# Kernel tuning notes

Measured on AMD Instinct MI355X. Metric: run time of the kernel, lower is better.

## Reference

```python
import jax, jax.numpy as jnp
import numpy as np

N_HEADS = 32
N_KV_HEADS = 8
HEAD_DIM = 128
ROPE_BASE = 10000.0
NEG_INF = -1e9


def rope(x, base=ROPE_BASE, offset=0):
    # x: [B, H, L, d]; 'traditional' RoPE with the module's rotation formula.
    d = x.shape[-1]
    t = jnp.arange(x.shape[2], dtype=jnp.float32) + offset
    freqs = base ** (-jnp.arange(0, d, 2, dtype=jnp.float32) / d)  # [d/2]
    ang = t[:, None] * freqs[None, :]                              # [L, d/2]
    cos, sin = jnp.cos(ang), jnp.sin(ang)
    x1, x2 = x[..., 0::2], x[..., 1::2]
    out = jnp.stack([x1 * cos + x2 * sin, x1 * sin - x2 * cos], axis=-1)
    return out.reshape(x.shape)


def setup_inputs() -> dict:
    key = jax.random.key(0)
    ks = jax.random.split(key, 5)
    B, L, D = 2, 2048, 4096
    x = jax.random.normal(ks[0], (B, L, D), dtype=jnp.float32)
    wq = jax.random.normal(ks[1], (D, N_HEADS * HEAD_DIM), dtype=jnp.float32) * 0.02
    wk = jax.random.normal(ks[2], (D, N_KV_HEADS * HEAD_DIM), dtype=jnp.float32) * 0.02
    wv = jax.random.normal(ks[3], (D, N_KV_HEADS * HEAD_DIM), dtype=jnp.float32) * 0.02
    wo = jax.random.normal(ks[4], (N_HEADS * HEAD_DIM, D), dtype=jnp.float32) * 0.02
    # causal additive mask [L, L]
    mask = jnp.where(jnp.tril(jnp.ones((L, L), dtype=bool)), 0.0, NEG_INF).astype(jnp.float32)
    return {"x": x, "mask": mask, "wq": wq, "wk": wk, "wv": wv, "wo": wo}


def reference(x, mask, wq, wk, wv, wo):
    B, L, D = x.shape
    scale = HEAD_DIM ** -0.5
    q = (x @ wq).reshape(B, L, N_HEADS, HEAD_DIM).transpose(0, 2, 1, 3)     # [B,H,L,d]
    k = (x @ wk).reshape(B, L, N_KV_HEADS, HEAD_DIM).transpose(0, 2, 1, 3)  # [B,Hk,L,d]
    v = (x @ wv).reshape(B, L, N_KV_HEADS, HEAD_DIM).transpose(0, 2, 1, 3)
    rep = N_HEADS // N_KV_HEADS
    k = jnp.repeat(k, rep, axis=1)  # [B,H,L,d]  (physical GQA repeat, as in source)
    v = jnp.repeat(v, rep, axis=1)
    q = rope(q)
    k = rope(k)
    scores = jnp.einsum("bhqd,bhkd->bhqk", q * scale, k) + mask  # [B,H,L,L]
    probs = jax.nn.softmax(scores.astype(jnp.float32), axis=-1).astype(scores.dtype)
    out = jnp.einsum("bhqk,bhkd->bhqd", probs, v)
    out = out.transpose(0, 2, 1, 3).reshape(B, L, N_HEADS * HEAD_DIM)
    return out @ wo, (k, v)
```

## Files before the change

kernel.cpp:

```cpp
#include <hip/hip_runtime.h>

typedef unsigned short u16;
typedef unsigned int u32;
typedef float f32x4 __attribute__((ext_vector_type(4)));
typedef u32 u32x2 __attribute__((ext_vector_type(2)));
typedef __bf16 bf16x8 __attribute__((ext_vector_type(8)));

#define DEV __device__ __forceinline__

DEV u16 f2b(float f) {
    union { float f; u32 u; } v; v.f = f;
    u32 r = v.u + 0x7fffu + ((v.u >> 16) & 1u);
    return (u16)(r >> 16);
}
DEV float b2f(u16 b) {
    union { u32 u; float f; } v; v.u = ((u32)b) << 16;
    return v.f;
}

DEV void gload16(const void* g, void* l) {
    __builtin_amdgcn_global_load_lds((const __attribute__((address_space(1))) void*)g,
                                     (__attribute__((address_space(3))) void*)l, 16, 0, 0);
}

DEV f32x4 mfma16(bf16x8 a, bf16x8 b, f32x4 c) {
    return __builtin_amdgcn_mfma_f32_16x16x32_bf16(a, b, c, 0, 0, 0);
}

__global__ __launch_bounds__(256) void convx_kernel(const float* __restrict__ in,
                                                    u16* __restrict__ out) {
    size_t i = ((size_t)blockIdx.x * 256 + threadIdx.x) * 4;
    float4 v = *(const float4*)(in + i);
    ushort4 o; o.x = f2b(v.x); o.y = f2b(v.y); o.z = f2b(v.z); o.w = f2b(v.w);
    *(ushort4*)(out + i) = o;
}

__global__ __launch_bounds__(256) void tconv_kernel(const float* __restrict__ in,
                                                    u16* __restrict__ out, int K, int N) {
    __shared__ float tile[64][65];
    int t = threadIdx.x;
    int n0 = blockIdx.x * 64, k0 = blockIdx.y * 64;
    int r = t >> 4, c4 = (t & 15) * 4;
#pragma unroll
    for (int i = 0; i < 4; ++i) {
        float4 v = *(const float4*)(in + (size_t)(k0 + i * 16 + r) * N + n0 + c4);
        tile[i * 16 + r][c4 + 0] = v.x; tile[i * 16 + r][c4 + 1] = v.y;
        tile[i * 16 + r][c4 + 2] = v.z; tile[i * 16 + r][c4 + 3] = v.w;
    }
    __syncthreads();
#pragma unroll
    for (int i = 0; i < 4; ++i) {
        int nn = i * 16 + r;
        ushort4 o;
        o.x = f2b(tile[c4 + 0][nn]); o.y = f2b(tile[c4 + 1][nn]);
        o.z = f2b(tile[c4 + 2][nn]); o.w = f2b(tile[c4 + 3][nn]);
        *(ushort4*)(out + (size_t)(n0 + nn) * K + k0 + c4) = o;
    }
}

template <bool F32OUT>
__global__ __launch_bounds__(256, 2) void gemm128_kernel(const u16* __restrict__ A,
                                                         const u16* __restrict__ Bt,
                                                         u16* __restrict__ Cb,
                                                         float* __restrict__ Cf,
                                                         int N, int K, int gy) {
    __shared__ __align__(16) u16 Asb[2][2][64 * 64];
    __shared__ __align__(16) u16 Bsb[2][2][64 * 64];
    int t = threadIdx.x;
    int lane = t & 63, w = t >> 6;
    int wrM = w >> 1, wcN = w & 1;
    int lr = lane & 15, hi = lane >> 4;
    int wg = blockIdx.x;
    int swz = (wg & 7) * ((int)gridDim.x >> 3) + (wg >> 3);
    int bx = swz / gy, by = swz % gy;
    int m0 = by * 128, n0 = bx * 128;
    int nk = K >> 6;

    auto stageA = [&](int X, int h) {
        const u16* src = A + (size_t)(m0 + h * 64) * K + X * 64;
        char* dst = (char*)&Asb[X & 1][h][0];
#pragma unroll
        for (int it = 0; it < 2; ++it) {
            int c = it * 256 + t;
            int row = c >> 3;
            int col8 = ((c & 7) ^ (row & 7)) << 3;
            gload16(src + (size_t)row * K + col8, dst + (it * 256 + (t & ~63)) * 16);
        }
    };
    auto stageB = [&](int X, int h) {
        const u16* src = Bt + (size_t)(n0 + h * 64) * K + X * 64;
        char* dst = (char*)&Bsb[X & 1][h][0];
#pragma unroll
        for (int it = 0; it < 2; ++it) {
            int c = it * 256 + t;
            int row = c >> 3;
            int col8 = ((c & 7) ^ (row & 7)) << 3;
            gload16(src + (size_t)row * K + col8, dst + (it * 256 + (t & ~63)) * 16);
        }
    };

    stageA(0, 0); stageA(0, 1); stageB(0, 0); stageB(0, 1);
    stageA(1, 0); stageA(1, 1);
    asm volatile("s_waitcnt vmcnt(4)" ::: "memory");
    __builtin_amdgcn_s_barrier();

    f32x4 acc[4][4] = {};
    for (int kt = 0; kt < nk; ++kt) {
        __builtin_amdgcn_sched_barrier(0);
        int p = kt & 1;
        const char* Ah = (const char*)&Asb[p][wrM][0];
        const char* Bh = (const char*)&Bsb[p][wcN][0];
        bool s1 = (kt + 1 < nk), s2 = (kt + 2 < nk);
        bf16x8 a[4][2], bb[2][2];

#pragma unroll
        for (int mf = 0; mf < 4; ++mf)
#pragma unroll
            for (int ks = 0; ks < 2; ++ks) {
                int row = mf * 16 + lr;
                a[mf][ks] = *(const bf16x8*)(Ah + ((row * 128 + ks * 64 + hi * 16) ^ ((row & 7) << 4)));
            }
#pragma unroll
        for (int nf = 0; nf < 2; ++nf)
#pragma unroll
            for (int ks = 0; ks < 2; ++ks) {
                int row = nf * 16 + lr;
                bb[nf][ks] = *(const bf16x8*)(Bh + ((row * 128 + ks * 64 + hi * 16) ^ ((row & 7) << 4)));
            }
        if (s1) { stageB(kt + 1, 0); stageB(kt + 1, 1); }
        __builtin_amdgcn_s_barrier();
        __builtin_amdgcn_s_setprio(1);
#pragma unroll
        for (int mf = 0; mf < 4; ++mf)
#pragma unroll
            for (int nf = 0; nf < 2; ++nf)
#pragma unroll
                for (int ks = 0; ks < 2; ++ks)
                    acc[mf][nf] = mfma16(a[mf][ks], bb[nf][ks], acc[mf][nf]);
        __builtin_amdgcn_s_setprio(0);
        __builtin_amdgcn_s_barrier();

#pragma unroll
        for (int nf = 0; nf < 2; ++nf)
#pragma unroll
            for (int ks = 0; ks < 2; ++ks) {
                int row = (nf + 2) * 16 + lr;
                bb[nf][ks] = *(const bf16x8*)(Bh + ((row * 128 + ks * 64 + hi * 16) ^ ((row & 7) << 4)));
            }
        if (s2) { stageA(kt + 2, 0); stageA(kt + 2, 1); }
        __builtin_amdgcn_s_barrier();
        __builtin_amdgcn_s_setprio(1);
#pragma unroll
        for (int mf = 0; mf < 4; ++mf)
#pragma unroll
            for (int nf = 0; nf < 2; ++nf)
#pragma unroll
                for (int ks = 0; ks < 2; ++ks)
                    acc[mf][nf + 2] = mfma16(a[mf][ks], bb[nf][ks], acc[mf][nf + 2]);
        __builtin_amdgcn_s_setprio(0);
        if (s2)      asm volatile("s_waitcnt vmcnt(4)" ::: "memory");
        else if (s1) asm volatile("s_waitcnt vmcnt(0)" ::: "memory");
        __builtin_amdgcn_s_barrier();
    }

#pragma unroll
    for (int mf = 0; mf < 4; ++mf)
#pragma unroll
        for (int nf = 0; nf < 4; ++nf)
#pragma unroll
            for (int r = 0; r < 4; ++r) {
                int m = m0 + wrM * 64 + mf * 16 + hi * 4 + r;
                int n = n0 + wcN * 64 + nf * 16 + lr;
                if (F32OUT) Cf[(size_t)m * N + n] = acc[mf][nf][r];
                else        Cb[(size_t)m * N + n] = f2b(acc[mf][nf][r]);
            }
}

__global__ __launch_bounds__(256) void rope_kernel(u16* __restrict__ qkv,
                                                   float* __restrict__ outk) {
    int row = blockIdx.y;
    int p = blockIdx.x * 256 + threadIdx.x;
    int b = row >> 11, l = row & 2047;
    float freq = exp2f((float)(p & 63) * -0.2076205059304601f);
    float sv, cv; sincosf((float)l * freq, &sv, &cv);
    if (p < 2048) {
        int h = p >> 6, i = p & 63;
        size_t idx = (size_t)row * 6144 + h * 128 + 2 * i;
        u32 pr = *(const u32*)(qkv + idx);
        float x1 = b2f((u16)(pr & 0xffff)), x2 = b2f((u16)(pr >> 16));
        float o1 = x1 * cv + x2 * sv, o2 = x1 * sv - x2 * cv;
        *(u32*)(qkv + idx) = (u32)f2b(o1) | ((u32)f2b(o2) << 16);
    } else {
        int kvh = (p >> 6) - 32, i = p & 63;
        size_t idx = (size_t)row * 6144 + 4096 + kvh * 128 + 2 * i;
        u32 pr = *(const u32*)(qkv + idx);
        float x1 = b2f((u16)(pr & 0xffff)), x2 = b2f((u16)(pr >> 16));
        float o1 = x1 * cv + x2 * sv, o2 = x1 * sv - x2 * cv;
        *(u32*)(qkv + idx) = (u32)f2b(o1) | ((u32)f2b(o2) << 16);
#pragma unroll
        for (int r = 0; r < 4; ++r) {
            float2 o; o.x = o1; o.y = o2;
            *(float2*)(outk + ((size_t)((b * 32 + kvh * 4 + r) * 2048) + l) * 128 + 2 * i) = o;
        }
    }
}

__global__ __launch_bounds__(256) void vtrans_kernel(const u16* __restrict__ qkv,
                                                     u16* __restrict__ vt,
                                                     float* __restrict__ outv) {
    __shared__ u16 tile[64][65];
    int t = threadIdx.x;
    int l0 = blockIdx.x * 64, d0 = blockIdx.y * 64;
    int z = blockIdx.z, b = z >> 3, kvh = z & 7;
    int r = t >> 4, c4 = (t & 15) * 4;
#pragma unroll
    for (int i = 0; i < 4; ++i) {
        int l = l0 + i * 16 + r;
        ushort4 v = *(const ushort4*)(qkv + (size_t)(b * 2048 + l) * 6144 + 5120 + kvh * 128 + d0 + c4);
        tile[i * 16 + r][c4 + 0] = v.x; tile[i * 16 + r][c4 + 1] = v.y;
        tile[i * 16 + r][c4 + 2] = v.z; tile[i * 16 + r][c4 + 3] = v.w;
        float4 f; f.x = b2f(v.x); f.y = b2f(v.y); f.z = b2f(v.z); f.w = b2f(v.w);
#pragma unroll
        for (int rr = 0; rr < 4; ++rr)
            *(float4*)(outv + ((size_t)((b * 32 + kvh * 4 + rr) * 2048) + l) * 128 + d0 + c4) = f;
    }
    __syncthreads();
#pragma unroll
    for (int i = 0; i < 4; ++i) {
        int dn = i * 16 + r;
        ushort4 o;
        o.x = tile[c4 + 0][dn]; o.y = tile[c4 + 1][dn];
        o.z = tile[c4 + 2][dn]; o.w = tile[c4 + 3][dn];
        *(ushort4*)(vt + (size_t)((b * 8 + kvh) * 128 + d0 + dn) * 2048 + l0 + c4) = o;
    }
}

__global__ __launch_bounds__(256, 2) void attn_kernel(const u16* __restrict__ qkv,
                                                      const u16* __restrict__ vt,
                                                      u16* __restrict__ ab) {
    __shared__ __align__(16) u16 Kbuf[2][64 * 128];
    __shared__ __align__(16) u16 Vbuf[2][128 * 64];
    __shared__ __align__(16) u16 Ps[4][32 * 64];
    int t = threadIdx.x, lane = t & 63, w = t >> 6;
    int lr = lane & 15, hi = lane >> 4;
    int h = blockIdx.y, b = blockIdx.z, kvh = h >> 2;

    const u16* kbase = qkv + (size_t)(b * 2048) * 6144 + 4096 + kvh * 128;
    const u16* vtbase = vt + (size_t)((b * 8 + kvh) * 128) * 2048;

    auto stageKV = [&](int k0, int buf) {
#pragma unroll
        for (int i = 0; i < 4; ++i) {
            int c = i * 256 + t;
            int row = c >> 4;
            int col8 = ((c & 15) ^ (row & 7)) << 3;
            gload16(kbase + (size_t)(k0 + row) * 6144 + col8,
                    (char*)Kbuf[buf] + (i * 256 + (t & ~63)) * 16);
        }
#pragma unroll
        for (int i = 0; i < 4; ++i) {
            int c = i * 256 + t;
            int row = c >> 3;
            int col8 = ((c & 7) ^ (row & 7)) << 3;
            gload16(vtbase + (size_t)row * 2048 + k0 + col8,
                    (char*)Vbuf[buf] + (i * 256 + (t & ~63)) * 16);
        }
    };

    auto process = [&](int qblk) {
        int q0 = qblk * 128;
        bf16x8 qf[2][4];
#pragma unroll
        for (int half = 0; half < 2; ++half)
#pragma unroll
            for (int kki = 0; kki < 4; ++kki)
                qf[half][kki] = *(const bf16x8*)(qkv +
                    (size_t)(b * 2048 + q0 + w * 32 + half * 16 + lr) * 6144 + h * 128 +
                    kki * 32 + 8 * hi);
        f32x4 acc[2][8] = {};
        float mrun[2] = {-1e30f, -1e30f}, lrun[2] = {0.f, 0.f};

        int nt = 2 * (qblk + 1);
        stageKV(0, 0);
        __syncthreads();
        int cur = 0;
        for (int kt = 0; kt < nt; ++kt) {
            if (kt + 1 < nt) stageKV((kt + 1) * 64, cur ^ 1);
            __builtin_amdgcn_sched_barrier(0);

            const u16* Ks = Kbuf[cur];
            const u16* Vs = Vbuf[cur];
            f32x4 s[2][4] = {};
            __builtin_amdgcn_s_setprio(1);
#pragma unroll
            for (int kki = 0; kki < 4; ++kki) {
                bf16x8 kf[4];
#pragma unroll
                for (int fc = 0; fc < 4; ++fc) {
                    int kvr = fc * 16 + lr;
                    int byt = (kvr * 256 + (kki * 32 + 8 * hi) * 2) ^ ((kvr & 7) << 4);
                    kf[fc] = *(const bf16x8*)((const char*)Ks + byt);
                }
#pragma unroll
                for (int fc = 0; fc < 4; ++fc) {
                    s[0][fc] = mfma16(kf[fc], qf[0][kki], s[0][fc]);
                    s[1][fc] = mfma16(kf[fc], qf[1][kki], s[1][fc]);
                }
            }
            __builtin_amdgcn_s_setprio(0);
            const float SC = 0.08838834764831845f;
            int domask = (kt >= nt - 2);
            u16* Pw = Ps[w];
#pragma unroll
            for (int half = 0; half < 2; ++half) {
                int qabs = q0 + w * 32 + half * 16 + lr;
#pragma unroll
                for (int fc = 0; fc < 4; ++fc)
#pragma unroll
                    for (int r = 0; r < 4; ++r) {
                        float v = s[half][fc][r] * SC;
                        if (domask && (kt * 64 + fc * 16 + hi * 4 + r) > qabs) v = -1e30f;
                        s[half][fc][r] = v;
                    }
                float pm = s[half][0][0];
#pragma unroll
                for (int fc = 0; fc < 4; ++fc)
#pragma unroll
                    for (int r = 0; r < 4; ++r) pm = fmaxf(pm, s[half][fc][r]);
                pm = fmaxf(pm, __shfl_xor(pm, 16));
                pm = fmaxf(pm, __shfl_xor(pm, 32));
                float mn = fmaxf(mrun[half], pm);
                float fr = __expf(mrun[half] - mn);
                mrun[half] = mn;
                float ls = 0.f;
#pragma unroll
                for (int fc = 0; fc < 4; ++fc)
#pragma unroll
                    for (int r = 0; r < 4; ++r) {
                        float e = __expf(s[half][fc][r] - mn);
                        s[half][fc][r] = e;
                        ls += e;
                    }
                ls += __shfl_xor(ls, 16);
                ls += __shfl_xor(ls, 32);
                lrun[half] = lrun[half] * fr + ls;
#pragma unroll
                for (int dhf = 0; dhf < 8; ++dhf)
#pragma unroll
                    for (int r = 0; r < 4; ++r) acc[half][dhf][r] *= fr;
#pragma unroll
                for (int fc = 0; fc < 4; ++fc) {
                    u32x2 pk;
                    pk.x = (u32)f2b(s[half][fc][0]) | ((u32)f2b(s[half][fc][1]) << 16);
                    pk.y = (u32)f2b(s[half][fc][2]) | ((u32)f2b(s[half][fc][3]) << 16);
                    int byt = (half * 2048 + lr * 128 + fc * 32 + hi * 8) ^ ((lr & 7) << 4);
                    *(u32x2*)((char*)Pw + byt) = pk;
                }
            }
            asm volatile("s_waitcnt lgkmcnt(0)" ::: "memory");
            __builtin_amdgcn_s_setprio(1);
#pragma unroll
            for (int kk2 = 0; kk2 < 2; ++kk2) {
                bf16x8 pf0 = *(const bf16x8*)((const char*)Pw +
                    ((lr * 128 + kk2 * 64 + hi * 16) ^ ((lr & 7) << 4)));
                bf16x8 pf1 = *(const bf16x8*)((const char*)Pw +
                    ((2048 + lr * 128 + kk2 * 64 + hi * 16) ^ ((lr & 7) << 4)));
#pragma unroll
                for (int dhf = 0; dhf < 8; ++dhf) {
                    int dh = dhf * 16 + lr;
                    int bytv = (dh * 128 + (kk2 * 32 + 8 * hi) * 2) ^ ((dh & 7) << 4);
                    bf16x8 vf = *(const bf16x8*)((const char*)Vs + bytv);
                    acc[0][dhf] = mfma16(vf, pf0, acc[0][dhf]);
                    acc[1][dhf] = mfma16(vf, pf1, acc[1][dhf]);
                }
            }
            __builtin_amdgcn_s_setprio(0);
            __syncthreads();
            cur ^= 1;
        }
#pragma unroll
        for (int half = 0; half < 2; ++half) {
            float inv = 1.0f / lrun[half];
            int qrow = q0 + w * 32 + half * 16 + lr;
#pragma unroll
            for (int dhf = 0; dhf < 8; ++dhf) {
                ushort4 o;
                o.x = f2b(acc[half][dhf][0] * inv); o.y = f2b(acc[half][dhf][1] * inv);
                o.z = f2b(acc[half][dhf][2] * inv); o.w = f2b(acc[half][dhf][3] * inv);
                *(ushort4*)(ab + (size_t)(b * 2048 + qrow) * 4096 + h * 128 + dhf * 16 + hi * 4) = o;
            }
        }
    };

    process(15 - blockIdx.x);
    __syncthreads();
    process(blockIdx.x);
}

extern "C" void kernel_launch(void* const* d_in, const int* in_sizes, int n_in,
                              void* d_out, int out_size, void* d_ws, size_t ws_size,
                              hipStream_t stream) {
    (void)in_sizes; (void)n_in; (void)out_size; (void)ws_size;
    const float* x  = (const float*)d_in[0];
    const float* wq = (const float*)d_in[2];
    const float* wk = (const float*)d_in[3];
    const float* wv = (const float*)d_in[4];
    const float* wo = (const float*)d_in[5];

    char* ws = (char*)d_ws;
    u16* xb  = (u16*)(ws + 0);
    u16* fBt = (u16*)(ws + 33554432);
    u16* qkv = (u16*)(ws + 83886080);
    u16* vt  = (u16*)(ws + 134217728);
    u16* ab  = xb;
    u16* wob = fBt;

    float* out0 = (float*)d_out;
    float* outk = out0 + 16777216;
    float* outv = out0 + 33554432;

    convx_kernel<<<16384, 256, 0, stream>>>(x, xb);
    tconv_kernel<<<dim3(64, 64), 256, 0, stream>>>(wq, fBt, 4096, 4096);
    tconv_kernel<<<dim3(16, 64), 256, 0, stream>>>(wk, fBt + (size_t)4096 * 4096, 4096, 1024);
    tconv_kernel<<<dim3(16, 64), 256, 0, stream>>>(wv, fBt + (size_t)5120 * 4096, 4096, 1024);

    gemm128_kernel<false><<<1536, 256, 0, stream>>>(xb, fBt, qkv, nullptr, 6144, 4096, 32);

    tconv_kernel<<<dim3(64, 64), 256, 0, stream>>>(wo, wob, 4096, 4096);

    rope_kernel<<<dim3(10, 4096), 256, 0, stream>>>(qkv, outk);
    vtrans_kernel<<<dim3(32, 2, 16), 256, 0, stream>>>(qkv, vt, outv);

    attn_kernel<<<dim3(8, 32, 2), 256, 0, stream>>>(qkv, vt, ab);

    gemm128_kernel<true><<<1024, 256, 0, stream>>>(ab, wob, nullptr, out0, 4096, 4096, 32);
}
```

Before: 581.0 us.

## Fuse RoPE and K-cache output into QKV GEMM epilogue

Removes the standalone RoPE kernel by applying the rotation in the QKV GEMM epilogue, using a lane shuffle to pair adjacent columns. The same epilogue also writes the repeated fp32 K output. This saves a full read/write pass over the qkv buffer and one kernel launch. In exchange it adds per-element sincos in the epilogue and scalar scattered stores for K.

Result: slower. 606.2 us (+4.3%).

```diff
diff --git a/kernel.cpp b/kernel.cpp
--- a/kernel.cpp
+++ b/kernel.cpp
@@ -58,111 +58,145 @@
     }
 }
 
-template <bool F32OUT>
+#define GEMM128_BODY                                                                        \
+    __shared__ __align__(16) u16 Asb[2][2][64 * 64];                                        \
+    __shared__ __align__(16) u16 Bsb[2][2][64 * 64];                                        \
+    int t = threadIdx.x;                                                                    \
+    int lane = t & 63, w = t >> 6;                                                          \
+    int wrM = w >> 1, wcN = w & 1;                                                          \
+    int lr = lane & 15, hi = lane >> 4;                                                     \
+    int wg = blockIdx.x;                                                                    \
+    int swz = (wg & 7) * ((int)gridDim.x >> 3) + (wg >> 3);                                 \
+    int bx = swz / gy, by = swz % gy;                                                       \
+    int m0 = by * 128, n0 = bx * 128;                                                       \
+    int nk = K >> 6;                                                                        \
+    auto stageA = [&](int X, int h) {                                                       \
+        const u16* src = A + (size_t)(m0 + h * 64) * K + X * 64;                            \
+        char* dst = (char*)&Asb[X & 1][h][0];                                               \
+        _Pragma("unroll")                                                                   \
+        for (int it = 0; it < 2; ++it) {                                                    \
+            int c = it * 256 + t;                                                           \
+            int row = c >> 3;                                                               \
+            int col8 = ((c & 7) ^ (row & 7)) << 3;                                          \
+            gload16(src + (size_t)row * K + col8, dst + (it * 256 + (t & ~63)) * 16);       \
+        }                                                                                   \
+    };                                                                                      \
+    auto stageB = [&](int X, int h) {                                                       \
+        const u16* src = Bt + (size_t)(n0 + h * 64) * K + X * 64;                           \
+        char* dst = (char*)&Bsb[X & 1][h][0];                                               \
+        _Pragma("unroll")                                                                   \
+        for (int it = 0; it < 2; ++it) {                                                    \
+            int c = it * 256 + t;                                                           \
+            int row = c >> 3;                                                               \
+            int col8 = ((c & 7) ^ (row & 7)) << 3;                                          \
+            gload16(src + (size_t)row * K + col8, dst + (it * 256 + (t & ~63)) * 16);       \
+        }                                                                                   \
+    };                                                                                      \
+    stageA(0, 0); stageA(0, 1); stageB(0, 0); stageB(0, 1);                                 \
+    stageA(1, 0); stageA(1, 1);                                                             \
+    asm volatile("s_waitcnt vmcnt(4)" ::: "memory");                                        \
+    __builtin_amdgcn_s_barrier();                                                           \
+    f32x4 acc[4][4] = {};                                                                   \
+    for (int kt = 0; kt < nk; ++kt) {                                                       \
+        __builtin_amdgcn_sched_barrier(0);                                                  \
+        int p = kt & 1;                                                                     \
+        const char* Ah = (const char*)&Asb[p][wrM][0];                                      \
+        const char* Bh = (const char*)&Bsb[p][wcN][0];                                      \
+        bool s1 = (kt + 1 < nk), s2 = (kt + 2 < nk);                                        \
+        bf16x8 a[4][2], bb[2][2];                                                           \
+        _Pragma("unroll")                                                                   \
+        for (int mf = 0; mf < 4; ++mf)                                                      \
+            _Pragma("unroll")                                                               \
+            for (int ks = 0; ks < 2; ++ks) {                                                \
+                int row = mf * 16 + lr;                                                     \
+                a[mf][ks] = *(const bf16x8*)(Ah + ((row * 128 + ks * 64 + hi * 16) ^ ((row & 7) << 4))); \
+            }                                                                               \
+        _Pragma("unroll")                                                                   \
+        for (int nf = 0; nf < 2; ++nf)                                                      \
+            _Pragma("unroll")                                                               \
+            for (int ks = 0; ks < 2; ++ks) {                                                \
+                int row = nf * 16 + lr;                                                     \
+                bb[nf][ks] = *(const bf16x8*)(Bh + ((row * 128 + ks * 64 + hi * 16) ^ ((row & 7) << 4))); \
+            }                                                                               \
+        if (s1) { stageB(kt + 1, 0); stageB(kt + 1, 1); }                                   \
+        __builtin_amdgcn_s_barrier();                                                       \
+        __builtin_amdgcn_s_setprio(1);                                                      \
+        _Pragma("unroll")                                                                   \
+        for (int mf = 0; mf < 4; ++mf)                                                      \
+            _Pragma("unroll")                                                               \
+            for (int nf = 0; nf < 2; ++nf)                                                  \
+                _Pragma("unroll")                                                           \
+                for (int ks = 0; ks < 2; ++ks)                                              \
+                    acc[mf][nf] = mfma16(a[mf][ks], bb[nf][ks], acc[mf][nf]);               \
+        __builtin_amdgcn_s_setprio(0);                                                      \
+        __builtin_amdgcn_s_barrier();                                                       \
+        _Pragma("unroll")                                                                   \
+        for (int nf = 0; nf < 2; ++nf)                                                      \
+            _Pragma("unroll")                                                               \
+            for (int ks = 0; ks < 2; ++ks) {                                                \
+                int row = (nf + 2) * 16 + lr;                                               \
+                bb[nf][ks] = *(const bf16x8*)(Bh + ((row * 128 + ks * 64 + hi * 16) ^ ((row & 7) << 4))); \
+            }                                                                               \
+        if (s2) { stageA(kt + 2, 0); stageA(kt + 2, 1); }                                   \
+        __builtin_amdgcn_s_barrier();                                                       \
+        __builtin_amdgcn_s_setprio(1);                                                      \
+        _Pragma("unroll")                                                                   \
+        for (int mf = 0; mf < 4; ++mf)                                                      \
+            _Pragma("unroll")                                                               \
+            for (int nf = 0; nf < 2; ++nf)                                                  \
+                _Pragma("unroll")                                                           \
+                for (int ks = 0; ks < 2; ++ks)                                              \
+                    acc[mf][nf + 2] = mfma16(a[mf][ks], bb[nf][ks], acc[mf][nf + 2]);       \
+        __builtin_amdgcn_s_setprio(0);                                                      \
+        if (s2)      asm volatile("s_waitcnt vmcnt(4)" ::: "memory");                       \
+        else if (s1) asm volatile("s_waitcnt vmcnt(0)" ::: "memory");                       \
+        __builtin_amdgcn_s_barrier();                                                       \
+    }
+
+__global__ __launch_bounds__(256, 2) void gemm128_qkv_kernel(const u16* __restrict__ A,
+                                                             const u16* __restrict__ Bt,
+                                                             u16* __restrict__ Cb,
+                                                             float* __restrict__ outk,
+                                                             int N, int K, int gy) {
+    GEMM128_BODY
+    int isv = (n0 >= 5120);
+    int isk = (n0 >= 4096) && !isv;
+    int odd = lane & 1;
+#pragma unroll
+    for (int nf = 0; nf < 4; ++nf) {
+        int n = n0 + wcN * 64 + nf * 16 + lr;
+        int d = n & 127;
+        float freq = exp2f((float)(d >> 1) * -0.2076205059304601f);
+#pragma unroll
+        for (int mf = 0; mf < 4; ++mf)
+#pragma unroll
+            for (int r = 0; r < 4; ++r) {
+                int m = m0 + wrM * 64 + mf * 16 + hi * 4 + r;
+                int l = m & 2047, bi = m >> 11;
+                float val = acc[mf][nf][r];
+                float pair = __shfl_xor(val, 1);
+                float out = val;
+                if (!isv) {
+                    float sv, cv;
+                    sincosf((float)l * freq, &sv, &cv);
+                    out = odd ? (pair * sv - val * cv) : (val * cv + pair * sv);
+                }
+                Cb[(size_t)m * N + n] = f2b(out);
+                if (isk) {
+                    int kvh = (n - 4096) >> 7;
+#pragma unroll
+                    for (int rr = 0; rr < 4; ++rr)
+                        outk[((size_t)((bi * 32 + kvh * 4 + rr) * 2048) + l) * 128 + d] = out;
+                }
+            }
+    }
+}
+
 __global__ __launch_bounds__(256, 2) void gemm128_kernel(const u16* __restrict__ A,
                                                          const u16* __restrict__ Bt,
-                                                         u16* __restrict__ Cb,
                                                          float* __restrict__ Cf,
                                                          int N, int K, int gy) {
-    __shared__ __align__(16) u16 Asb[2][2][64 * 64];
-    __shared__ __align__(16) u16 Bsb[2][2][64 * 64];
-    int t = threadIdx.x;
-    int lane = t & 63, w = t >> 6;
-    int wrM = w >> 1, wcN = w & 1;
-    int lr = lane & 15, hi = lane >> 4;
-    int wg = blockIdx.x;
-    int swz = (wg & 7) * ((int)gridDim.x >> 3) + (wg >> 3);
-    int bx = swz / gy, by = swz % gy;
-    int m0 = by * 128, n0 = bx * 128;
-    int nk = K >> 6;
-
-    auto stageA = [&](int X, int h) {
-        const u16* src = A + (size_t)(m0 + h * 64) * K + X * 64;
-        char* dst = (char*)&Asb[X & 1][h][0];
-#pragma unroll
-        for (int it = 0; it < 2; ++it) {
-            int c = it * 256 + t;
-            int row = c >> 3;
-            int col8 = ((c & 7) ^ (row & 7)) << 3;
-            gload16(src + (size_t)row * K + col8, dst + (it * 256 + (t & ~63)) * 16);
-        }
-    };
-    auto stageB = [&](int X, int h) {
-        const u16* src = Bt + (size_t)(n0 + h * 64) * K + X * 64;
-        char* dst = (char*)&Bsb[X & 1][h][0];
-#pragma unroll
-        for (int it = 0; it < 2; ++it) {
-            int c = it * 256 + t;
-            int row = c >> 3;
-            int col8 = ((c & 7) ^ (row & 7)) << 3;
-            gload16(src + (size_t)row * K + col8, dst + (it * 256 + (t & ~63)) * 16);
-        }
-    };
-
-    stageA(0, 0); stageA(0, 1); stageB(0, 0); stageB(0, 1);
-    stageA(1, 0); stageA(1, 1);
-    asm volatile("s_waitcnt vmcnt(4)" ::: "memory");
-    __builtin_amdgcn_s_barrier();
-
-    f32x4 acc[4][4] = {};
-    for (int kt = 0; kt < nk; ++kt) {
-        __builtin_amdgcn_sched_barrier(0);
-        int p = kt & 1;
-        const char* Ah = (const char*)&Asb[p][wrM][0];
-        const char* Bh = (const char*)&Bsb[p][wcN][0];
-        bool s1 = (kt + 1 < nk), s2 = (kt + 2 < nk);
-        bf16x8 a[4][2], bb[2][2];
-
-#pragma unroll
-        for (int mf = 0; mf < 4; ++mf)
-#pragma unroll
-            for (int ks = 0; ks < 2; ++ks) {
-                int row = mf * 16 + lr;
-                a[mf][ks] = *(const bf16x8*)(Ah + ((row * 128 + ks * 64 + hi * 16) ^ ((row & 7) << 4)));
-            }
-#pragma unroll
-        for (int nf = 0; nf < 2; ++nf)
-#pragma unroll
-            for (int ks = 0; ks < 2; ++ks) {
-                int row = nf * 16 + lr;
-                bb[nf][ks] = *(const bf16x8*)(Bh + ((row * 128 + ks * 64 + hi * 16) ^ ((row & 7) << 4)));
-            }
-        if (s1) { stageB(kt + 1, 0); stageB(kt + 1, 1); }
-        __builtin_amdgcn_s_barrier();
-        __builtin_amdgcn_s_setprio(1);
-#pragma unroll
-        for (int mf = 0; mf < 4; ++mf)
-#pragma unroll
-            for (int nf = 0; nf < 2; ++nf)
-#pragma unroll
-                for (int ks = 0; ks < 2; ++ks)
-                    acc[mf][nf] = mfma16(a[mf][ks], bb[nf][ks], acc[mf][nf]);
-        __builtin_amdgcn_s_setprio(0);
-        __builtin_amdgcn_s_barrier();
-
-#pragma unroll
-        for (int nf = 0; nf < 2; ++nf)
-#pragma unroll
-            for (int ks = 0; ks < 2; ++ks) {
-                int row = (nf + 2) * 16 + lr;
-                bb[nf][ks] = *(const bf16x8*)(Bh + ((row * 128 + ks * 64 + hi * 16) ^ ((row & 7) << 4)));
-            }
-        if (s2) { stageA(kt + 2, 0); stageA(kt + 2, 1); }
-        __builtin_amdgcn_s_barrier();
-        __builtin_amdgcn_s_setprio(1);
-#pragma unroll
-        for (int mf = 0; mf < 4; ++mf)
-#pragma unroll
-            for (int nf = 0; nf < 2; ++nf)
-#pragma unroll
-                for (int ks = 0; ks < 2; ++ks)
-                    acc[mf][nf + 2] = mfma16(a[mf][ks], bb[nf][ks], acc[mf][nf + 2]);
-        __builtin_amdgcn_s_setprio(0);
-        if (s2)      asm volatile("s_waitcnt vmcnt(4)" ::: "memory");
-        else if (s1) asm volatile("s_waitcnt vmcnt(0)" ::: "memory");
-        __builtin_amdgcn_s_barrier();
-    }
-
+    GEMM128_BODY
 #pragma unroll
     for (int mf = 0; mf < 4; ++mf)
 #pragma unroll
@@ -171,38 +205,8 @@
             for (int r = 0; r < 4; ++r) {
                 int m = m0 + wrM * 64 + mf * 16 + hi * 4 + r;
                 int n = n0 + wcN * 64 + nf * 16 + lr;
-                if (F32OUT) Cf[(size_t)m * N + n] = acc[mf][nf][r];
-                else        Cb[(size_t)m * N + n] = f2b(acc[mf][nf][r]);
-            }
-}
-
-__global__ __launch_bounds__(256) void rope_kernel(u16* __restrict__ qkv,
-                                                   float* __restrict__ outk) {
-    int row = blockIdx.y;
-    int p = blockIdx.x * 256 + threadIdx.x;
-    int b = row >> 11, l = row & 2047;
-    float freq = exp2f((float)(p & 63) * -0.2076205059304601f);
-    float sv, cv; sincosf((float)l * freq, &sv, &cv);
-    if (p < 2048) {
-        int h = p >> 6, i = p & 63;
-        size_t idx = (size_t)row * 6144 + h * 128 + 2 * i;
-        u32 pr = *(const u32*)(qkv + idx);
-        float x1 = b2f((u16)(pr & 0xffff)), x2 = b2f((u16)(pr >> 16));
-        float o1 = x1 * cv + x2 * sv, o2 = x1 * sv - x2 * cv;
-        *(u32*)(qkv + idx) = (u32)f2b(o1) | ((u32)f2b(o2) << 16);
-    } else {
-        int kvh = (p >> 6) - 32, i = p & 63;
-        size_t idx = (size_t)row * 6144 + 4096 + kvh * 128 + 2 * i;
-        u32 pr = *(const u32*)(qkv + idx);
-        float x1 = b2f((u16)(pr & 0xffff)), x2 = b2f((u16)(pr >> 16));
-        float o1 = x1 * cv + x2 * sv, o2 = x1 * sv - x2 * cv;
-        *(u32*)(qkv + idx) = (u32)f2b(o1) | ((u32)f2b(o2) << 16);
-#pragma unroll
-        for (int r = 0; r < 4; ++r) {
-            float2 o; o.x = o1; o.y = o2;
-            *(float2*)(outk + ((size_t)((b * 32 + kvh * 4 + r) * 2048) + l) * 128 + 2 * i) = o;
-        }
-    }
+                Cf[(size_t)m * N + n] = acc[mf][nf][r];
+            }
 }
 
 __global__ __launch_bounds__(256) void vtrans_kernel(const u16* __restrict__ qkv,
@@ -424,14 +428,13 @@
     tconv_kernel<<<dim3(16, 64), 256, 0, stream>>>(wk, fBt + (size_t)4096 * 4096, 4096, 1024);
     tconv_kernel<<<dim3(16, 64), 256, 0, stream>>>(wv, fBt + (size_t)5120 * 4096, 4096, 1024);
 
-    gemm128_kernel<false><<<1536, 256, 0, stream>>>(xb, fBt, qkv, nullptr, 6144, 4096, 32);
+    gemm128_qkv_kernel<<<1536, 256, 0, stream>>>(xb, fBt, qkv, outk, 6144, 4096, 32);
 
     tconv_kernel<<<dim3(64, 64), 256, 0, stream>>>(wo, wob, 4096, 4096);
 
-    rope_kernel<<<dim3(10, 4096), 256, 0, stream>>>(qkv, outk);
     vtrans_kernel<<<dim3(32, 2, 16), 256, 0, stream>>>(qkv, vt, outv);
 
     attn_kernel<<<dim3(8, 32, 2), 256, 0, stream>>>(qkv, vt, ab);
 
-    gemm128_kernel<true><<<1024, 256, 0, stream>>>(ab, wob, nullptr, out0, 4096, 4096, 32);
-}
+    gemm128_kernel<<<1024, 256, 0, stream>>>(ab, wob, out0, 4096, 4096, 32);
+}
```
